# Kernel tuning notes

Measured on AMD Instinct MI355X. Metric: run time of the kernel, lower is better.

## Reference

```python
import jax, jax.numpy as jnp
import numpy as np

B, C, H, W, R = 8, 256, 64, 64, 16


def setup_inputs() -> dict:
    key = jax.random.key(0)
    ks = jax.random.split(key, 14)
    def w(k, shape, fan):
        return (jax.random.normal(k, shape, jnp.float32) / np.sqrt(fan)).astype(jnp.float32)
    return {
        "features_depth": jax.random.normal(ks[0], (B, C, H, W), jnp.float32),
        "features_semseg": jax.random.normal(ks[1], (B, C, H, W), jnp.float32),
        "W0": w(ks[2], (C, 2 * C), 2 * C),          # conv_split0 1x1, [out,in]
        "Wdw": w(ks[3], (C, 1, 3, 3), 9),            # depthwise 3x3, groups=C
        "Wq": w(ks[4], (C, C), C),                   # Linear weights [out,in]
        "Wk": w(ks[5], (C, C), C),
        "Wv": w(ks[6], (C, C), C),
        "Wp": w(ks[7], (C, C), C),
        "bp": jnp.zeros((C,), jnp.float32),
        "Wsplit": w(ks[8], (C, C), C),               # conv_split 1x1
        "se_d_w1": w(ks[9], (C // R, C), C),         # SE squeeze conv1x1 (depth)
        "se_d_w2": w(ks[10], (C, C // R), C // R),
        "se_s_w1": w(ks[11], (C // R, C), C),        # SE squeeze conv1x1 (semseg)
        "se_s_w2": w(ks[12], (C, C // R), C // R),
    }


def _l2norm(a, eps=1e-12):
    n = jnp.linalg.norm(a, axis=-1, keepdims=True)
    return a / jnp.maximum(n, eps)


def _se(x, w1, w2):
    # x: [B,C,H,W]; global avg pool -> 1x1 convs -> sigmoid gate
    p = x.mean(axis=(2, 3))                                  # [B,C]
    h = jax.nn.relu(jnp.einsum('rc,bc->br', w1, p))          # [B,C/R]
    g = jax.nn.sigmoid(jnp.einsum('cr,br->bc', w2, h))       # [B,C]
    return x * g[:, :, None, None]


def reference(features_depth, features_semseg, W0, Wdw, Wq, Wk, Wv, Wp, bp,
              Wsplit, se_d_w1, se_d_w2, se_s_w1, se_s_w2):
    x = jnp.concatenate([features_depth, features_semseg], axis=1)  # [B,2C,H,W]
    x = jnp.einsum('oc,bchw->bohw', W0, x)                          # 1x1 conv
    x = jax.lax.conv_general_dilated(
        x, Wdw, window_strides=(1, 1), padding='SAME',
        dimension_numbers=('NCHW', 'OIHW', 'NCHW'), feature_group_count=C)
    xt = x.transpose(0, 2, 3, 1).reshape(B, H * W, C)               # [B,N,C]
    q = (xt @ Wq.T).transpose(0, 2, 1)                              # [B,C,N]
    k = (xt @ Wk.T).transpose(0, 2, 1)
    v = (xt @ Wv.T).transpose(0, 2, 1)
    q = _l2norm(q)
    k = _l2norm(k)
    attn = jax.nn.softmax(jnp.einsum('bcn,bdn->bcd', k, q), axis=-1)  # [B,C,C]
    y = jnp.einsum('bcd,bdn->bcn', attn, v)                         # [B,C,N]
    y = y.transpose(0, 2, 1)                                        # [B,N,C]
    y = y @ Wp.T + bp                                               # proj
    out_c = y.reshape(B, H, W, C).transpose(0, 3, 1, 2)             # [B,C,H,W]
    out_c = jnp.einsum('oc,bchw->bohw', Wsplit, out_c)              # 1x1 conv
    out_depth = _se(out_c, se_d_w1, se_d_w2) + features_depth
    out_semseg = _se(out_c, se_s_w1, se_s_w2) + features_semseg
    return (out_depth, out_semseg)
```

## Files before the change

kernel.cpp:

```cpp
#include <hip/hip_runtime.h>
#include <cstdint>

#define DEVI __device__ __forceinline__

using fx4 = __attribute__((ext_vector_type(4))) float;
using bf8 = __attribute__((ext_vector_type(8))) __bf16;
using s8v = __attribute__((ext_vector_type(8))) short;
using s4v = __attribute__((ext_vector_type(4))) short;
typedef unsigned short u16;
typedef unsigned int u32;

DEVI float b2f(u16 u) { return __builtin_bit_cast(float, (u32)u << 16); }
DEVI u16 f2b(float f) {
  u32 u = __builtin_bit_cast(u32, f);
  return (u16)((u + 0x7fffu + ((u >> 16) & 1u)) >> 16);
}

#define GLOAD(g, l)                                                          \
  __builtin_amdgcn_global_load_lds(                                          \
      (const __attribute__((address_space(1))) unsigned int*)(g),            \
      (__attribute__((address_space(3))) unsigned int*)(l), 16, 0, 0)

__global__ __launch_bounds__(256) void prep(const float* __restrict__ W0,
                                            const float* __restrict__ Wq,
                                            const float* __restrict__ Wk,
                                            const float* __restrict__ Wv,
                                            u16* __restrict__ w0b,
                                            u16* __restrict__ wqk2,
                                            u16* __restrict__ wvtb) {
  const int i = blockIdx.x * 256 + threadIdx.x;
  if (blockIdx.y == 0) {
    if (i < 131072) w0b[i] = f2b(W0[i]);
  } else if (blockIdx.y == 1) {
    if (i < 524288) {
      const int row = i >> 9, c = i & 511;
      const float* src = (row < 256) ? Wq : Wk;
      wqk2[i] = f2b(src[((row & 255) << 8) + (c & 255)]);
    }
  } else {
    if (i < 65536) {
      const int e = i >> 8, d = i & 255;
      wvtb[i] = f2b(Wv[d * 256 + e]);
    }
  }
}

__global__ __launch_bounds__(256) void wcmul(const float* __restrict__ Wsp,
                                             const float* __restrict__ Wp,
                                             const float* __restrict__ bp,
                                             u16* __restrict__ wcb, float* __restrict__ bc) {
  const int o = blockIdx.x, t = threadIdx.x;
  __shared__ float row[256];
  __shared__ float red[4];
  row[t] = Wsp[o * 256 + t];
  __syncthreads();
  float acc = 0.f;
  for (int c = 0; c < 256; ++c) acc += row[c] * Wp[c * 256 + t];
  wcb[o * 256 + t] = f2b(acc);
  float pb = row[t] * bp[t];
#pragma unroll
  for (int m = 32; m > 0; m >>= 1) pb += __shfl_xor(pb, m);
  if ((t & 63) == 0) red[t >> 6] = pb;
  __syncthreads();
  if (t == 0) bc[o] = red[0] + red[1] + red[2] + red[3];
}

__global__ void pack_cat(const float* __restrict__ fd, const float* __restrict__ fs,
                         u16* __restrict__ out) {
  __shared__ float t[32][33];
  const int b = blockIdx.z;
  const int n0 = blockIdx.x * 32;
  const int g = blockIdx.y;
  const float* src = (g < 8) ? fd : fs;
  const int c0 = (g & 7) * 32;
  const int ccol0 = g * 32;
  const int tx = threadIdx.x;
  const int ty = threadIdx.y;
  const float* sp = src + ((long)b * 256 + c0) * 4096 + n0;
#pragma unroll
  for (int i = 0; i < 4; ++i) {
    int c = ty + i * 8;
    t[c][tx] = sp[(long)c * 4096 + tx];
  }
  __syncthreads();
  u16* op = out + ((long)b * 4096 + n0) * 512 + ccol0;
#pragma unroll
  for (int i = 0; i < 4; ++i) {
    int r = ty + i * 8;
    op[(long)r * 512 + tx] = f2b(t[tx][r]);
  }
}

template <typename OT, int BIAS, bool POOL, int EPI>
__global__ __launch_bounds__(256) void gemm_nt(
    const u16* __restrict__ A, long sA, int lda,
    const u16* __restrict__ B, long sB, int ldb,
    OT* __restrict__ C, long sC, long sCs, int ldc,
    const float* __restrict__ bias, int Keff, int ksplit,
    float* __restrict__ poolpart,
    const float* __restrict__ wqf, const float* __restrict__ wkf,
    float* __restrict__ dpart) {
  __shared__ u16 ldsA[128 * 64];
  __shared__ u16 ldsB[128 * 64];
  const int z = blockIdx.z;
  const int bb = z / ksplit;
  const int ss = z - bb * ksplit;
  const int bm = blockIdx.x * 128;
  const int bn = blockIdx.y * 128;
  const u16* Ab = A + bb * sA + (long)ss * Keff + (long)bm * lda;
  const u16* Bb = B + bb * sB + (long)ss * Keff + (long)bn * ldb;
  const int tid = threadIdx.x;
  const int wid = tid >> 6;
  const int lane = tid & 63;
  const int wm = wid >> 1, wn = wid & 1;
  const int srow = tid >> 3;
  const int slot = tid & 7;

  fx4 acc[4][4] = {};
  for (int kt = 0; kt < Keff; kt += 64) {
#pragma unroll
    for (int i = 0; i < 4; ++i) {
      const int row = i * 32 + srow;
      const int kq = slot ^ (row & 7);
      GLOAD(Ab + (long)row * lda + kt + kq * 8, &ldsA[i * 2048 + wid * 512]);
      GLOAD(Bb + (long)row * ldb + kt + kq * 8, &ldsB[i * 2048 + wid * 512]);
    }
    __syncthreads();
#pragma unroll
    for (int ko = 0; ko < 2; ++ko) {
      bf8 af[4], bfr[4];
      const int kq = ko * 4 + (lane >> 4);
#pragma unroll
      for (int f = 0; f < 4; ++f) {
        const int ar = wm * 64 + f * 16 + (lane & 15);
        af[f] = *(const bf8*)&ldsA[ar * 64 + ((kq ^ (ar & 7)) * 8)];
        const int br = wn * 64 + f * 16 + (lane & 15);
        bfr[f] = *(const bf8*)&ldsB[br * 64 + ((kq ^ (br & 7)) * 8)];
      }
#pragma unroll
      for (int fm = 0; fm < 4; ++fm)
#pragma unroll
        for (int fn = 0; fn < 4; ++fn)
          acc[fm][fn] = __builtin_amdgcn_mfma_f32_16x16x32_bf16(af[fm], bfr[fn], acc[fm][fn], 0, 0, 0);
    }
    __syncthreads();
  }
  if constexpr (EPI == 1) {
    u16* S2b = (u16*)C + bb * sC;
    float dp[4][4];
#pragma unroll
    for (int fm = 0; fm < 4; ++fm)
#pragma unroll
      for (int r = 0; r < 4; ++r) dp[fm][r] = 0.f;
#pragma unroll
    for (int fm = 0; fm < 4; ++fm) {
      const int m0 = bm + wm * 64 + fm * 16 + ((lane >> 4) << 2);
#pragma unroll
      for (int fn = 0; fn < 4; ++fn) {
        const int n0 = bn + wn * 64 + fn * 16 + (lane & 15);
#pragma unroll
        for (int r = 0; r < 4; ++r) {
          const float v = acc[fm][fn][r];
          const int m = m0 + r;
          if (m < 256) {
            const u16 hi = f2b(v);
            S2b[(long)m * 512 + n0] = hi;
            S2b[(long)m * 512 + 256 + n0] = f2b(v - b2f(hi));
          }
          const float* wr = (m < 256) ? (wqf + (long)m * 256) : (wkf + (long)(m - 256) * 256);
          dp[fm][r] += v * wr[n0];
        }
      }
    }
#pragma unroll
    for (int fm = 0; fm < 4; ++fm)
#pragma unroll
      for (int r = 0; r < 4; ++r) {
        float s = dp[fm][r];
        s += __shfl_xor(s, 1); s += __shfl_xor(s, 2);
        s += __shfl_xor(s, 4); s += __shfl_xor(s, 8);
        if ((lane & 15) == 0) {
          const int m = bm + wm * 64 + fm * 16 + ((lane >> 4) << 2) + r;
          dpart[(long)(blockIdx.y * 2 + wn) * 4096 + bb * 512 + m] = s;
        }
      }
    return;
  }
  OT* Cb = C + bb * sC + ss * sCs;
  float pr[4][4];
  if (POOL) {
#pragma unroll
    for (int fm = 0; fm < 4; ++fm)
#pragma unroll
      for (int r = 0; r < 4; ++r) pr[fm][r] = 0.f;
  }
#pragma unroll
  for (int fm = 0; fm < 4; ++fm) {
    const int m0 = bm + wm * 64 + fm * 16 + ((lane >> 4) << 2);
#pragma unroll
    for (int fn = 0; fn < 4; ++fn) {
      const int n0 = bn + wn * 64 + fn * 16 + (lane & 15);
#pragma unroll
      for (int r = 0; r < 4; ++r) {
        float v = acc[fm][fn][r];
        if (BIAS == 2) v += bias[m0 + r];
        if constexpr (sizeof(OT) == 2) Cb[(long)(m0 + r) * ldc + n0] = (OT)f2b(v);
        else Cb[(long)(m0 + r) * ldc + n0] = v;
        if (POOL) pr[fm][r] += v;
      }
    }
  }
  if (POOL) {
#pragma unroll
    for (int fm = 0; fm < 4; ++fm)
#pragma unroll
      for (int r = 0; r < 4; ++r) {
        float s = pr[fm][r];
        s += __shfl_xor(s, 1); s += __shfl_xor(s, 2);
        s += __shfl_xor(s, 4); s += __shfl_xor(s, 8);
        if ((lane & 15) == 0) {
          const int o = bm + wm * 64 + fm * 16 + ((lane >> 4) << 2) + r;
          poolpart[(long)(blockIdx.y * 2 + wn) * 2048 + bb * 256 + o] = s;
        }
      }
  }
}

__global__ __launch_bounds__(256) void dwconv2(const u16* __restrict__ x,
                                               const float* __restrict__ wdw,
                                               u16* __restrict__ y,
                                               u16* __restrict__ yT) {
  __shared__ float wsm[9][256];
  __shared__ u16 tb[256][72];
  const int t = threadIdx.x;
  for (int i = t; i < 2304; i += 256) wsm[i % 9][i / 9] = wdw[i];
  const int b = blockIdx.x >> 6, h = blockIdx.x & 63;
  const int c8 = (t & 31) * 8, wsub = t >> 5;
  const u16* base = x + ((long)b << 20);
  __syncthreads();
#pragma unroll
  for (int i = 0; i < 8; ++i) {
    const int w = wsub + 8 * i;
    float acc[8] = {0.f, 0.f, 0.f, 0.f, 0.f, 0.f, 0.f, 0.f};
#pragma unroll
    for (int ky = 0; ky < 3; ++ky) {
      const int hy = h + ky - 1;
      if ((unsigned)hy >= 64u) continue;
#pragma unroll
      for (int kx = 0; kx < 3; ++kx) {
        const int wx = w + kx - 1;
        if ((unsigned)wx >= 64u) continue;
        const s8v v = *(const s8v*)&base[(((hy << 6) + wx) << 8) + c8];
        const int kk = ky * 3 + kx;
        const fx4 wa = *(const fx4*)&wsm[kk][c8];
        const fx4 wb = *(const fx4*)&wsm[kk][c8 + 4];
#pragma unroll
        for (int j = 0; j < 4; ++j) {
          acc[j] += wa[j] * b2f((u16)v[j]);
          acc[4 + j] += wb[j] * b2f((u16)v[4 + j]);
        }
      }
    }
    s8v o;
#pragma unroll
    for (int j = 0; j < 8; ++j) o[j] = (short)f2b(acc[j]);
    *(s8v*)&y[((long)b << 20) + (long)(((h << 6) + w) << 8) + c8] = o;
#pragma unroll
    for (int j = 0; j < 8; ++j) tb[c8 + j][w] = (u16)o[j];
  }
  __syncthreads();
  u16* dst = yT + ((long)b << 20) + (long)t * 4096 + (h << 6);
#pragma unroll
  for (int j = 0; j < 8; ++j)
    *(s8v*)&dst[j * 8] = *(const s8v*)&tb[t][j * 8];
}

__global__ __launch_bounds__(256) void gsplit(const float* __restrict__ part,
                                              u16* __restrict__ G2) {
  const int i4 = (blockIdx.x * 256 + threadIdx.x) * 4;
  fx4 s = {0.f, 0.f, 0.f, 0.f};
#pragma unroll
  for (int ss = 0; ss < 4; ++ss) s += *(const fx4*)(part + (long)ss * 524288 + i4);
  const int b = i4 >> 16, rem = i4 & 65535, e = rem >> 8, c0 = rem & 255;
  u16* d = G2 + (long)b * 131072 + (long)e * 512 + c0;
  s4v hi, lo;
#pragma unroll
  for (int j = 0; j < 4; ++j) {
    u16 h = f2b(s[j]);
    hi[j] = (short)h;
    lo[j] = (short)f2b(s[j] - b2f(h));
  }
  *(s4v*)d = hi;
  *(s4v*)(d + 256) = lo;
}

__global__ __launch_bounds__(256) void softmax_g2(const float* __restrict__ araw,
                                                  const float* __restrict__ dpart,
                                                  u16* __restrict__ out) {
  const int wid = threadIdx.x >> 6, lane = threadIdx.x & 63;
  const int t = threadIdx.x;
  const int b = blockIdx.x >> 6;
  __shared__ float rq[256];
  float dq = dpart[b * 512 + t] + dpart[4096 + b * 512 + t] +
             dpart[8192 + b * 512 + t] + dpart[12288 + b * 512 + t];
  rq[t] = 1.f / fmaxf(sqrtf(fmaxf(dq, 0.f)), 1e-12f);
  __syncthreads();
  const long row = (long)blockIdx.x * 4 + wid;
  const int c = (int)(row & 255);
  const int ki = b * 512 + 256 + c;
  float dk = dpart[ki] + dpart[4096 + ki] + dpart[8192 + ki] + dpart[12288 + ki];
  const float rk = 1.f / fmaxf(sqrtf(fmaxf(dk, 0.f)), 1e-12f);
  fx4 v = ((const fx4*)(araw + row * 256))[lane];
  v[0] *= rk * rq[lane * 4];     v[1] *= rk * rq[lane * 4 + 1];
  v[2] *= rk * rq[lane * 4 + 2]; v[3] *= rk * rq[lane * 4 + 3];
  float m = fmaxf(fmaxf(v[0], v[1]), fmaxf(v[2], v[3]));
#pragma unroll
  for (int o = 32; o > 0; o >>= 1) m = fmaxf(m, __shfl_xor(m, o));
  float e0 = __expf(v[0] - m), e1 = __expf(v[1] - m);
  float e2 = __expf(v[2] - m), e3 = __expf(v[3] - m);
  float s4 = e0 + e1 + e2 + e3;
#pragma unroll
  for (int o = 32; o > 0; o >>= 1) s4 += __shfl_xor(s4, o);
  const float inv = 1.f / s4;
  u16* op = out + row * 256 + lane * 4;
  op[0] = f2b(e0 * inv); op[1] = f2b(e1 * inv);
  op[2] = f2b(e2 * inv); op[3] = f2b(e3 * inv);
}

__global__ __launch_bounds__(256) void se_gates(const float* __restrict__ poolpart,
                                                const float* __restrict__ w1d, const float* __restrict__ w2d,
                                                const float* __restrict__ w1s, const float* __restrict__ w2s,
                                                float* __restrict__ gd, float* __restrict__ gs) {
  const int b = blockIdx.x;
  const int t = threadIdx.x;
  __shared__ float p[256], hd[16], hs[16];
  float s = 0.f;
#pragma unroll 8
  for (int sl = 0; sl < 64; ++sl) s += poolpart[(long)sl * 2048 + b * 256 + t];
  p[t] = s * (1.f / 4096.f);
  __syncthreads();
  if (t < 16) {
    float ad = 0.f, as2 = 0.f;
    for (int j = 0; j < 256; ++j) {
      ad += w1d[t * 256 + j] * p[j];
      as2 += w1s[t * 256 + j] * p[j];
    }
    hd[t] = fmaxf(ad, 0.f);
    hs[t] = fmaxf(as2, 0.f);
  }
  __syncthreads();
  float ad = 0.f, as2 = 0.f;
#pragma unroll
  for (int r = 0; r < 16; ++r) {
    ad += w2d[t * 16 + r] * hd[r];
    as2 += w2s[t * 16 + r] * hs[r];
  }
  gd[b * 256 + t] = 1.f / (1.f + __expf(-ad));
  gs[b * 256 + t] = 1.f / (1.f + __expf(-as2));
}

__global__ __launch_bounds__(256) void fuse_out2(const u16* __restrict__ oc,
                                                 const u16* __restrict__ cat,
                                                 const float* __restrict__ gd,
                                                 const float* __restrict__ gs,
                                                 float* __restrict__ od,
                                                 float* __restrict__ os) {
  __shared__ u16 td[32][68];
  __shared__ u16 ts2[32][68];
  const int b = blockIdx.z;
  const int c0 = blockIdx.y * 32;
  const int n0 = blockIdx.x * 64;
  const int t = threadIdx.x;
  {
    const int n = t >> 2, cj = (t & 3) * 8;
    const u16* cb = cat + ((long)b * 4096 + n0 + n) * 512 + c0 + cj;
    const s8v vd = *(const s8v*)cb;
    const s8v vs = *(const s8v*)(cb + 256);
#pragma unroll
    for (int j = 0; j < 8; ++j) {
      td[cj + j][n] = (u16)vd[j];
      ts2[cj + j][n] = (u16)vs[j];
    }
  }
  __syncthreads();
  const int c = t >> 3, no = (t & 7) * 8;
  const long obase = ((long)b * 256 + c0 + c) * 4096 + n0 + no;
  const float gdv = gd[b * 256 + c0 + c];
  const float gsv = gs[b * 256 + c0 + c];
  const s8v o8 = *(const s8v*)&oc[obase];
  fx4 r0, r1, q0, q1;
#pragma unroll
  for (int j = 0; j < 4; ++j) {
    const float vl = b2f((u16)o8[j]);
    const float vh = b2f((u16)o8[4 + j]);
    r0[j] = vl * gdv + b2f(td[c][no + j]);
    r1[j] = vh * gdv + b2f(td[c][no + 4 + j]);
    q0[j] = vl * gsv + b2f(ts2[c][no + j]);
    q1[j] = vh * gsv + b2f(ts2[c][no + 4 + j]);
  }
  *(fx4*)(od + obase) = r0; *(fx4*)(od + obase + 4) = r1;
  *(fx4*)(os + obase) = q0; *(fx4*)(os + obase + 4) = q1;
}

extern "C" void kernel_launch(void* const* d_in, const int* in_sizes, int n_in,
                              void* d_out, int out_size, void* d_ws, size_t ws_size,
                              hipStream_t stream) {
  const float* fd  = (const float*)d_in[0];
  const float* fs  = (const float*)d_in[1];
  const float* W0  = (const float*)d_in[2];
  const float* Wdw = (const float*)d_in[3];
  const float* Wq  = (const float*)d_in[4];
  const float* Wk  = (const float*)d_in[5];
  const float* Wv  = (const float*)d_in[6];
  const float* Wp  = (const float*)d_in[7];
  const float* bp  = (const float*)d_in[8];
  const float* Wsp = (const float*)d_in[9];
  const float* w1d = (const float*)d_in[10];
  const float* w2d = (const float*)d_in[11];
  const float* w1s = (const float*)d_in[12];
  const float* w2s = (const float*)d_in[13];

  char* ws = (char*)d_ws;
  u16* catb   = (u16*)(ws + 0);
  u16* x0b    = (u16*)(ws + 33554432);
  u16* outcb  = x0b;
  u16* xtb    = (u16*)(ws + 50331648);
  u16* xtT    = (u16*)(ws + 67108864);
  float* part = (float*)(ws + 83886080);
  u16* G2     = (u16*)(ws + 92274688);
  u16* S2     = (u16*)(ws + 94371840);
  float* araw = (float*)(ws + 96468992);
  u16* attnb  = (u16*)(ws + 98566144);
  u16* m1t    = (u16*)(ws + 99614720);
  u16* wfin   = (u16*)(ws + 100663296);
  u16* w0b    = (u16*)(ws + 101711872);
  u16* wqk2   = (u16*)(ws + 101974016);
  u16* wvtb   = (u16*)(ws + 102498304);
  u16* wcb    = (u16*)(ws + 102629376);
  float* bcb  = (float*)(ws + 102760448);
  float* dpart = (float*)(ws + 102761472);
  float* poolpart = (float*)(ws + 102827008);
  float* gdp  = (float*)(ws + 103351296);
  float* gsp  = (float*)(ws + 103359488);
  float* od  = (float*)d_out;
  float* osg = od + 8388608;

  prep<<<dim3(2048, 3), 256, 0, stream>>>(W0, Wq, Wk, Wv, w0b, wqk2, wvtb);
  wcmul<<<256, 256, 0, stream>>>(Wsp, Wp, bp, wcb, bcb);
  pack_cat<<<dim3(128, 16, 8), dim3(32, 8), 0, stream>>>(fd, fs, catb);
  gemm_nt<u16, 0, false, 0><<<dim3(32, 2, 8), 256, 0, stream>>>(
      catb, 2097152, 512, w0b, 0, 512, x0b, 1048576, 0, 256, nullptr, 512, 1,
      nullptr, nullptr, nullptr, nullptr);
  dwconv2<<<512, 256, 0, stream>>>(x0b, Wdw, xtb, xtT);
  gemm_nt<float, 0, false, 0><<<dim3(2, 2, 32), 256, 0, stream>>>(
      xtT, 1048576, 4096, xtT, 1048576, 4096,
      part, 65536, 524288, 256, nullptr, 1024, 4, nullptr, nullptr, nullptr, nullptr);
  gsplit<<<512, 256, 0, stream>>>(part, G2);
  gemm_nt<u16, 0, false, 1><<<dim3(4, 2, 8), 256, 0, stream>>>(
      wqk2, 0, 512, G2, 131072, 512, S2, 131072, 0, 512, nullptr, 512, 1,
      nullptr, Wq, Wk, dpart);
  gemm_nt<float, 0, false, 0><<<dim3(2, 2, 8), 256, 0, stream>>>(
      wqk2 + 131072, 0, 512, S2, 131072, 512, araw, 65536, 0, 256, nullptr, 512, 1,
      nullptr, nullptr, nullptr, nullptr);
  softmax_g2<<<512, 256, 0, stream>>>(araw, dpart, attnb);
  gemm_nt<u16, 0, false, 0><<<dim3(2, 2, 8), 256, 0, stream>>>(
      wvtb, 0, 256, attnb, 65536, 256, m1t, 65536, 0, 256, nullptr, 256, 1,
      nullptr, nullptr, nullptr, nullptr);
  gemm_nt<u16, 0, false, 0><<<dim3(2, 2, 8), 256, 0, stream>>>(
      wcb, 0, 256, m1t, 65536, 256, wfin, 65536, 0, 256, nullptr, 256, 1,
      nullptr, nullptr, nullptr, nullptr);
  gemm_nt<u16, 2, true, 0><<<dim3(2, 32, 8), 256, 0, stream>>>(
      wfin, 65536, 256, xtb, 1048576, 256, outcb, 1048576, 0, 4096, bcb, 256, 1,
      poolpart, nullptr, nullptr, nullptr);
  se_gates<<<8, 256, 0, stream>>>(poolpart, w1d, w2d, w1s, w2s, gdp, gsp);
  fuse_out2<<<dim3(64, 8, 8), 256, 0, stream>>>(outcb, catb, gdp, gsp, od, osg);
}
```

Baseline: 198.4 us.

## Split dwconv into per-pixel kernel plus separate transpose; double Gram split-K

Result: faster. 182.8 us (-7.9%).

```diff
diff --git a/kernel.cpp b/kernel.cpp
--- a/kernel.cpp
+++ b/kernel.cpp
@@ -226,53 +226,66 @@
   }
 }
 
-__global__ __launch_bounds__(256) void dwconv2(const u16* __restrict__ x,
-                                               const float* __restrict__ wdw,
-                                               u16* __restrict__ y,
-                                               u16* __restrict__ yT) {
-  __shared__ float wsm[9][256];
-  __shared__ u16 tb[256][72];
+__global__ __launch_bounds__(256) void dwconv3x3(const u16* __restrict__ x,
+                                                 const float* __restrict__ wdw,
+                                                 u16* __restrict__ y) {
+  __shared__ float w[9][256];
   const int t = threadIdx.x;
-  for (int i = t; i < 2304; i += 256) wsm[i % 9][i / 9] = wdw[i];
-  const int b = blockIdx.x >> 6, h = blockIdx.x & 63;
-  const int c8 = (t & 31) * 8, wsub = t >> 5;
+  for (int i = t; i < 2304; i += 256) w[i % 9][i / 9] = wdw[i];
+  __syncthreads();
+  const int nb = blockIdx.x;
+  const int b = nb >> 9;
+  const int n0 = (nb & 511) << 3;
+  const int tn = t >> 5;
+  const int tc = (t & 31) << 3;
+  const int n = n0 + tn;
+  const int hh = n >> 6, ww2 = n & 63;
   const u16* base = x + ((long)b << 20);
-  __syncthreads();
-#pragma unroll
-  for (int i = 0; i < 8; ++i) {
-    const int w = wsub + 8 * i;
-    float acc[8] = {0.f, 0.f, 0.f, 0.f, 0.f, 0.f, 0.f, 0.f};
-#pragma unroll
-    for (int ky = 0; ky < 3; ++ky) {
-      const int hy = h + ky - 1;
-      if ((unsigned)hy >= 64u) continue;
-#pragma unroll
-      for (int kx = 0; kx < 3; ++kx) {
-        const int wx = w + kx - 1;
-        if ((unsigned)wx >= 64u) continue;
-        const s8v v = *(const s8v*)&base[(((hy << 6) + wx) << 8) + c8];
-        const int kk = ky * 3 + kx;
-        const fx4 wa = *(const fx4*)&wsm[kk][c8];
-        const fx4 wb = *(const fx4*)&wsm[kk][c8 + 4];
-#pragma unroll
-        for (int j = 0; j < 4; ++j) {
-          acc[j] += wa[j] * b2f((u16)v[j]);
-          acc[4 + j] += wb[j] * b2f((u16)v[4 + j]);
-        }
-      }
-    }
-    s8v o;
-#pragma unroll
-    for (int j = 0; j < 8; ++j) o[j] = (short)f2b(acc[j]);
-    *(s8v*)&y[((long)b << 20) + (long)(((h << 6) + w) << 8) + c8] = o;
-#pragma unroll
-    for (int j = 0; j < 8; ++j) tb[c8 + j][w] = (u16)o[j];
-  }
-  __syncthreads();
-  u16* dst = yT + ((long)b << 20) + (long)t * 4096 + (h << 6);
-#pragma unroll
-  for (int j = 0; j < 8; ++j)
-    *(s8v*)&dst[j * 8] = *(const s8v*)&tb[t][j * 8];
+  float acc[8] = {0.f, 0.f, 0.f, 0.f, 0.f, 0.f, 0.f, 0.f};
+#pragma unroll
+  for (int ky = 0; ky < 3; ++ky) {
+    const int hy = hh + ky - 1;
+    if ((unsigned)hy >= 64u) continue;
+#pragma unroll
+    for (int kx = 0; kx < 3; ++kx) {
+      const int wx = ww2 + kx - 1;
+      if ((unsigned)wx >= 64u) continue;
+      const s8v v = *(const s8v*)&base[(((hy << 6) + wx) << 8) + tc];
+      const int kk = ky * 3 + kx;
+      const fx4 wa = *(const fx4*)&w[kk][tc];
+      const fx4 wb = *(const fx4*)&w[kk][tc + 4];
+#pragma unroll
+      for (int j = 0; j < 4; ++j) {
+        acc[j] += wa[j] * b2f((u16)v[j]);
+        acc[4 + j] += wb[j] * b2f((u16)v[4 + j]);
+      }
+    }
+  }
+  s8v o;
+#pragma unroll
+  for (int j = 0; j < 8; ++j) o[j] = (short)f2b(acc[j]);
+  *(s8v*)&y[((long)b << 20) + ((long)n << 8) + tc] = o;
+}
+
+__global__ void btrans(const u16* __restrict__ x, u16* __restrict__ y) {
+  __shared__ u16 t[32][34];
+  const int b = blockIdx.z;
+  const int n0 = blockIdx.x * 32;
+  const int c0 = blockIdx.y * 32;
+  const int tx = threadIdx.x, ty = threadIdx.y;
+  const u16* sp = x + (long)b * 1048576 + (long)n0 * 256 + c0;
+#pragma unroll
+  for (int j = 0; j < 4; ++j) {
+    int i = ty + j * 8;
+    t[i][tx] = sp[(long)i * 256 + tx];
+  }
+  __syncthreads();
+  u16* op = y + (long)b * 1048576 + (long)c0 * 4096 + n0;
+#pragma unroll
+  for (int j = 0; j < 4; ++j) {
+    int r = ty + j * 8;
+    op[(long)r * 4096 + tx] = t[tx][r];
+  }
 }
 
 __global__ __launch_bounds__(256) void gsplit(const float* __restrict__ part,
@@ -280,7 +293,7 @@
   const int i4 = (blockIdx.x * 256 + threadIdx.x) * 4;
   fx4 s = {0.f, 0.f, 0.f, 0.f};
 #pragma unroll
-  for (int ss = 0; ss < 4; ++ss) s += *(const fx4*)(part + (long)ss * 524288 + i4);
+  for (int ss = 0; ss < 8; ++ss) s += *(const fx4*)(part + (long)ss * 524288 + i4);
   const int b = i4 >> 16, rem = i4 & 65535, e = rem >> 8, c0 = rem & 255;
   u16* d = G2 + (long)b * 131072 + (long)e * 512 + c0;
   s4v hi, lo;
@@ -427,21 +440,21 @@
   u16* xtb    = (u16*)(ws + 50331648);
   u16* xtT    = (u16*)(ws + 67108864);
   float* part = (float*)(ws + 83886080);
-  u16* G2     = (u16*)(ws + 92274688);
-  u16* S2     = (u16*)(ws + 94371840);
-  float* araw = (float*)(ws + 96468992);
-  u16* attnb  = (u16*)(ws + 98566144);
-  u16* m1t    = (u16*)(ws + 99614720);
-  u16* wfin   = (u16*)(ws + 100663296);
-  u16* w0b    = (u16*)(ws + 101711872);
-  u16* wqk2   = (u16*)(ws + 101974016);
-  u16* wvtb   = (u16*)(ws + 102498304);
-  u16* wcb    = (u16*)(ws + 102629376);
-  float* bcb  = (float*)(ws + 102760448);
-  float* dpart = (float*)(ws + 102761472);
-  float* poolpart = (float*)(ws + 102827008);
-  float* gdp  = (float*)(ws + 103351296);
-  float* gsp  = (float*)(ws + 103359488);
+  u16* G2     = (u16*)(ws + 100663296);
+  u16* S2     = (u16*)(ws + 102760448);
+  float* araw = (float*)(ws + 104857600);
+  u16* attnb  = (u16*)(ws + 106954752);
+  u16* m1t    = (u16*)(ws + 108003328);
+  u16* wfin   = (u16*)(ws + 109051904);
+  u16* w0b    = (u16*)(ws + 110100480);
+  u16* wqk2   = (u16*)(ws + 110362624);
+  u16* wvtb   = (u16*)(ws + 110886912);
+  u16* wcb    = (u16*)(ws + 111017984);
+  float* bcb  = (float*)(ws + 111149056);
+  float* dpart = (float*)(ws + 111150080);
+  float* poolpart = (float*)(ws + 111215616);
+  float* gdp  = (float*)(ws + 111739904);
+  float* gsp  = (float*)(ws + 111748096);
   float* od  = (float*)d_out;
   float* osg = od + 8388608;
 
@@ -451,10 +464,11 @@
   gemm_nt<u16, 0, false, 0><<<dim3(32, 2, 8), 256, 0, stream>>>(
       catb, 2097152, 512, w0b, 0, 512, x0b, 1048576, 0, 256, nullptr, 512, 1,
       nullptr, nullptr, nullptr, nullptr);
-  dwconv2<<<512, 256, 0, stream>>>(x0b, Wdw, xtb, xtT);
-  gemm_nt<float, 0, false, 0><<<dim3(2, 2, 32), 256, 0, stream>>>(
+  dwconv3x3<<<4096, 256, 0, stream>>>(x0b, Wdw, xtb);
+  btrans<<<dim3(128, 8, 8), dim3(32, 8), 0, stream>>>(xtb, xtT);
+  gemm_nt<float, 0, false, 0><<<dim3(2, 2, 64), 256, 0, stream>>>(
       xtT, 1048576, 4096, xtT, 1048576, 4096,
-      part, 65536, 524288, 256, nullptr, 1024, 4, nullptr, nullptr, nullptr, nullptr);
+      part, 65536, 524288, 256, nullptr, 512, 8, nullptr, nullptr, nullptr, nullptr);
   gsplit<<<512, 256, 0, stream>>>(part, G2);
   gemm_nt<u16, 0, false, 1><<<dim3(4, 2, 8), 256, 0, stream>>>(
       wqk2, 0, 512, G2, 131072, 512, S2, 131072, 0, 512, nullptr, 512, 1,
```
